# Kernel optimization log

Measured on AMD Instinct MI355X. Metric: run time of the kernel, lower is better.

## Reference

```python
import jax, jax.numpy as jnp
import numpy as np

THETA = 10000.0

def _rope_cos_sin(seq_len, head_dim, dtype=jnp.float32):
    # matches precompute_freqs_cis: freqs over even indices of head_dim
    inv = 1.0 / (THETA ** (jnp.arange(0, head_dim, 2, dtype=jnp.float32) / head_dim))  # [hd/2]
    ang = jnp.arange(seq_len, dtype=jnp.float32)[:, None] * inv[None, :]               # [S, hd/2]
    return jnp.cos(ang).astype(dtype), jnp.sin(ang).astype(dtype)

def _apply_rope(x, cos, sin):
    # x: [b, h, s, d]; pairs are interleaved (d r) with r=2 -> complex (even=real, odd=imag)
    xe = x[..., 0::2]
    xo = x[..., 1::2]
    re = xe * cos - xo * sin
    im = xe * sin + xo * cos
    # interleave back: [..., d/2, 2] -> [..., d]
    return jnp.stack([re, im], axis=-1).reshape(x.shape)

def setup_inputs() -> dict:
    key = jax.random.key(0)
    ks = jax.random.split(key, 8)
    B, S, D = 2, 2048, 1024
    s = 0.02
    return {
        "query": jax.random.normal(ks[0], (B, S, D), jnp.float32),
        "key": jax.random.normal(ks[1], (B, S, D), jnp.float32),
        "value": jax.random.normal(ks[2], (B, S, D), jnp.float32),
        "q_w": jax.random.normal(ks[3], (D, D), jnp.float32) * s,
        "q_b": jnp.zeros((D,), jnp.float32),
        "k_w": jax.random.normal(ks[4], (D, D), jnp.float32) * s,
        "k_b": jnp.zeros((D,), jnp.float32),
        "v_w": jax.random.normal(ks[5], (D, D), jnp.float32) * s,
        "v_b": jnp.zeros((D,), jnp.float32),
        "o_w": jax.random.normal(ks[6], (D, D), jnp.float32) * s,
        "o_b": jnp.zeros((D,), jnp.float32),
    }

def reference(query, key, value, q_w, q_b, k_w, k_b, v_w, v_b, o_w, o_b):
    H = 16
    B, S, D = query.shape
    hd = D // H
    scaling = hd ** -0.5

    def split_heads(x):  # [b, s, (h d)] -> [b, h, s, d]
        return x.reshape(B, -1, H, hd).transpose(0, 2, 1, 3)

    q = split_heads(query @ q_w.T + q_b)
    k = split_heads(key @ k_w.T + k_b)
    v = split_heads(value @ v_w.T + v_b)

    cos, sin = _rope_cos_sin(S, hd)
    q = _apply_rope(q, cos, sin)
    k = _apply_rope(k, cos, sin)

    scores = jnp.einsum('bhqd,bhkd->bhqk', q, k) * scaling  # [B,H,S,S]
    attn = jax.nn.softmax(scores, axis=-1)
    out = jnp.einsum('bhqk,bhkd->bhqd', attn, v)            # [B,H,S,hd]
    out = out.transpose(0, 2, 1, 3).reshape(B, S, D)
    return out @ o_w.T + o_b
```

## Files before the change

kernel.cpp:

```cpp
#include <hip/hip_runtime.h>
#include <math.h>

#define B_  2
#define S_  2048
#define D_  1024
#define H_  16
#define HD_ 64
#define M_  (B_*S_)

typedef __attribute__((ext_vector_type(8))) short bf16x8;
typedef __attribute__((ext_vector_type(4))) float f32x4;
typedef unsigned short ushort_t;

#define MFMA32 __builtin_amdgcn_mfma_f32_16x16x32_bf16

__device__ inline unsigned short f2bf(float x) {
    unsigned u = __float_as_uint(x);
    unsigned r = (u + 0x7fff + ((u >> 16) & 1)) >> 16;
    return (unsigned short)r;
}
__device__ inline void gload16(const ushort_t* g, ushort_t* l) {
    __builtin_amdgcn_global_load_lds(
        (const __attribute__((address_space(1))) unsigned*)g,
        (__attribute__((address_space(3))) unsigned*)l, 16, 0, 0);
}

__global__ __launch_bounds__(256) void prep(
    const float* __restrict__ qa, const float* __restrict__ ka,
    const float* __restrict__ va,
    const float* __restrict__ qw, const float* __restrict__ kw,
    const float* __restrict__ vw, const float* __restrict__ ow,
    ushort_t* __restrict__ qab, ushort_t* __restrict__ kab,
    ushort_t* __restrict__ vab,
    ushort_t* __restrict__ qwb, ushort_t* __restrict__ kwb,
    ushort_t* __restrict__ vwb, ushort_t* __restrict__ owb,
    float* __restrict__ cost, float* __restrict__ sint)
{
    const int z = blockIdx.y;
    const int i = blockIdx.x * 256 + threadIdx.x;
    if (z == 7) {
        if (blockIdx.x >= (S_ * 32) / 256) return;
        int s = i >> 5, w = i & 31;
        double inv = pow(10000.0, -((double)(2 * w) / (double)HD_));
        double ang = (double)s * inv;
        cost[i] = (float)cos(ang);
        sint[i] = (float)sin(ang);
        return;
    }
    const float* in;
    ushort_t* dst;
    int n4;
    switch (z) {
        case 0: in = qa; dst = qab; n4 = (M_ * D_) / 4; break;
        case 1: in = ka; dst = kab; n4 = (M_ * D_) / 4; break;
        case 2: in = va; dst = vab; n4 = (M_ * D_) / 4; break;
        case 3: in = qw; dst = qwb; n4 = (D_ * D_) / 4; break;
        case 4: in = kw; dst = kwb; n4 = (D_ * D_) / 4; break;
        case 5: in = vw; dst = vwb; n4 = (D_ * D_) / 4; break;
        default: in = ow; dst = owb; n4 = (D_ * D_) / 4; break;
    }
    if (i >= n4) return;
    float4 v = ((const float4*)in)[i];
    unsigned short h0 = f2bf(v.x), h1 = f2bf(v.y), h2 = f2bf(v.z), h3 = f2bf(v.w);
    ((uint2*)dst)[i] = make_uint2((unsigned)h0 | ((unsigned)h1 << 16),
                                  (unsigned)h2 | ((unsigned)h3 << 16));
}

__global__ __launch_bounds__(256, 3) void fused_qkv(
    const ushort_t* __restrict__ A0, const ushort_t* __restrict__ A1,
    const ushort_t* __restrict__ A2,
    const ushort_t* __restrict__ W0, const ushort_t* __restrict__ W1,
    const ushort_t* __restrict__ W2,
    const float* __restrict__ b0, const float* __restrict__ b1,
    const float* __restrict__ b2,
    ushort_t* __restrict__ O0, ushort_t* __restrict__ O1,
    ushort_t* __restrict__ O2,
    const float* __restrict__ cost, const float* __restrict__ sint)
{
    __shared__ ushort_t Ab[8192];
    __shared__ ushort_t Wb[8192];

    const int tid  = threadIdx.x;
    const int wq   = tid >> 6;
    const int lane = tid & 63;
    const int l16  = lane & 15;
    const int quad = lane >> 4;
    const int bm   = blockIdx.y * 128;
    const int bn   = blockIdx.x * 128;
    const int z    = blockIdx.z;

    const ushort_t* A = z == 0 ? A0 : z == 1 ? A1 : A2;
    const ushort_t* W = z == 0 ? W0 : z == 1 ? W1 : W2;
    const float* bias = z == 0 ? b0 : z == 1 ? b1 : b2;

    const int m16 = tid & 15;
    const int akq = (tid >> 4) & 3;
    const int tw  = tid >> 6;

    const ushort_t* gA0 = A + (size_t)(bm + tw * 16 + m16) * D_ + akq * 8;
    const ushort_t* gA1 = gA0 + (size_t)64 * D_;
    const ushort_t* gW0 = W + (size_t)(bn + tw * 16 + m16) * D_ + akq * 8;
    const ushort_t* gW1 = gW0 + (size_t)64 * D_;

    const int wm = wq >> 1, wn = wq & 1;

    f32x4 acc[4][4];
#pragma unroll
    for (int mt = 0; mt < 4; ++mt)
#pragma unroll
        for (int nt = 0; nt < 4; ++nt)
            acc[mt][nt] = (f32x4){0.f, 0.f, 0.f, 0.f};

    gload16(gA0, &Ab[tw * 512]);
    gload16(gA1, &Ab[(tw + 4) * 512]);
    gload16(gW0, &Wb[tw * 512]);
    gload16(gW1, &Wb[(tw + 4) * 512]);
    __syncthreads();

    for (int k0 = 0; k0 < D_; k0 += 32) {
        const int cur = (k0 >> 5) & 1;
        if (k0 + 32 < D_) {
            const int nxt = cur ^ 1;
            gload16(gA0 + k0 + 32, &Ab[nxt * 4096 + tw * 512]);
            gload16(gA1 + k0 + 32, &Ab[nxt * 4096 + (tw + 4) * 512]);
            gload16(gW0 + k0 + 32, &Wb[nxt * 4096 + tw * 512]);
            gload16(gW1 + k0 + 32, &Wb[nxt * 4096 + (tw + 4) * 512]);
        }
        const ushort_t* Abc = &Ab[cur * 4096];
        const ushort_t* Wbc = &Wb[cur * 4096];

        bf16x8 af[4], wf[4];
#pragma unroll
        for (int mt = 0; mt < 4; ++mt)
            af[mt] = *(const bf16x8*)&Abc[(wm * 4 + mt) * 512 + lane * 8];
#pragma unroll
        for (int nt = 0; nt < 4; ++nt)
            wf[nt] = *(const bf16x8*)&Wbc[(wn * 4 + nt) * 512 + lane * 8];
#pragma unroll
        for (int mt = 0; mt < 4; ++mt)
#pragma unroll
            for (int nt = 0; nt < 4; ++nt)
                acc[mt][nt] = MFMA32(af[mt], wf[nt], acc[mt][nt], 0, 0, 0);
        __syncthreads();
    }

    if (z == 0) {
        const float scale = 0.18033688011112042f;
#pragma unroll
        for (int mt = 0; mt < 4; ++mt) {
            int m = bm + wm * 64 + mt * 16 + quad * 4;
#pragma unroll
            for (int nt = 0; nt < 4; ++nt) {
                int n = bn + wn * 64 + nt * 16 + l16;
                float bb = bias[n];
                int h = n >> 6, d = n & 63, p = d >> 1;
#pragma unroll
                for (int r = 0; r < 4; ++r) {
                    int mm = m + r;
                    int s = mm & (S_ - 1), b = mm >> 11;
                    float x = acc[mt][nt][r] + bb;
                    float cs = cost[s * 32 + p], sn = sint[s * 32 + p];
                    float part = __shfl_xor(x, 1);
                    float y = (d & 1) ? (part * sn + x * cs)
                                      : (x * cs - part * sn);
                    O0[((size_t)(b * H_ + h) * S_ + s) * HD_ + d] = f2bf(y * scale);
                }
            }
        }
    } else if (z == 1) {
#pragma unroll
        for (int mt = 0; mt < 4; ++mt) {
            int m = bm + wm * 64 + mt * 16 + quad * 4;
#pragma unroll
            for (int nt = 0; nt < 4; ++nt) {
                int n = bn + wn * 64 + nt * 16 + l16;
                float bb = bias[n];
                int h = n >> 6, d = n & 63, p = d >> 1;
                int sub = ((d >> 5) & 1);
                int dq  = (d >> 3) & 3;
                int dj  = d & 7;
#pragma unroll
                for (int r = 0; r < 4; ++r) {
                    int mm = m + r;
                    int s = mm & (S_ - 1), b = mm >> 11;
                    float x = acc[mt][nt][r] + bb;
                    float cs = cost[s * 32 + p], sn = sint[s * 32 + p];
                    float part = __shfl_xor(x, 1);
                    float y = (d & 1) ? (part * sn + x * cs)
                                      : (x * cs - part * sn);
                    int kt  = s >> 5;
                    int st  = ((s >> 4) & 1) * 2 + sub;
                    size_t idx = ((size_t)(b * H_ + h) * 64 + kt) * 2048
                               + st * 512 + dq * 128 + (s & 15) * 8 + dj;
                    O1[idx] = f2bf(y);
                }
            }
        }
    } else {
#pragma unroll
        for (int mt = 0; mt < 4; ++mt) {
            int m = bm + wm * 64 + mt * 16 + quad * 4;
            int b = m >> 11, s0 = m & (S_ - 1);
            int vt = s0 >> 5;
            int kk = s0 & 31;
            int qd = (kk & 15) >> 2;
            int w0 = ((kk >> 4) & 1) * 4;
#pragma unroll
            for (int nt = 0; nt < 4; ++nt) {
                int n = bn + wn * 64 + nt * 16 + l16;
                float bb = bias[n];
                int h = n >> 6, d = n & 63;
                int mtv = d >> 4, dd = d & 15;
                unsigned short hh[4];
#pragma unroll
                for (int r = 0; r < 4; ++r)
                    hh[r] = f2bf(acc[mt][nt][r] + bb);
                size_t idx = ((size_t)(b * H_ + h) * 64 + vt) * 2048
                           + mtv * 512 + qd * 128 + dd * 8 + w0;
                *(uint2*)(O2 + idx) = make_uint2(
                    (unsigned)hh[0] | ((unsigned)hh[1] << 16),
                    (unsigned)hh[2] | ((unsigned)hh[3] << 16));
            }
        }
    }
}

__global__ __launch_bounds__(256, 2) void proj_o(
    const ushort_t* __restrict__ A, const ushort_t* __restrict__ W,
    const float* __restrict__ bias, float* __restrict__ outf)
{
    __shared__ ushort_t Ab[4096];
    __shared__ ushort_t Wb[8192];

    const int tid  = threadIdx.x;
    const int wq   = tid >> 6;
    const int lane = tid & 63;
    const int l16  = lane & 15;
    const int quad = lane >> 4;
    const int bm   = blockIdx.y * 64;
    const int bn   = blockIdx.x * 128;

    const int m16 = tid & 15;
    const int akq = (tid >> 4) & 3;
    const int tw  = tid >> 6;

    const ushort_t* gA  = A + (size_t)(bm + tw * 16 + m16) * D_ + akq * 8;
    const ushort_t* gW0 = W + (size_t)(bn + tw * 16 + m16) * D_ + akq * 8;
    const ushort_t* gW1 = gW0 + (size_t)64 * D_;

    const int wm = wq >> 1, wn = wq & 1;

    f32x4 acc[2][4];
#pragma unroll
    for (int mt = 0; mt < 2; ++mt)
#pragma unroll
        for (int nt = 0; nt < 4; ++nt)
            acc[mt][nt] = (f32x4){0.f, 0.f, 0.f, 0.f};

    gload16(gA,  &Ab[tw * 512]);
    gload16(gW0, &Wb[tw * 512]);
    gload16(gW1, &Wb[(tw + 4) * 512]);
    __syncthreads();

    for (int k0 = 0; k0 < D_; k0 += 32) {
        const int cur = (k0 >> 5) & 1;
        if (k0 + 32 < D_) {
            const int nxt = cur ^ 1;
            gload16(gA  + k0 + 32, &Ab[nxt * 2048 + tw * 512]);
            gload16(gW0 + k0 + 32, &Wb[nxt * 4096 + tw * 512]);
            gload16(gW1 + k0 + 32, &Wb[nxt * 4096 + (tw + 4) * 512]);
        }
        const ushort_t* Abc = &Ab[cur * 2048];
        const ushort_t* Wbc = &Wb[cur * 4096];

        bf16x8 af[2], wf[4];
#pragma unroll
        for (int mt = 0; mt < 2; ++mt)
            af[mt] = *(const bf16x8*)&Abc[(wm * 2 + mt) * 512 + lane * 8];
#pragma unroll
        for (int nt = 0; nt < 4; ++nt)
            wf[nt] = *(const bf16x8*)&Wbc[(wn * 4 + nt) * 512 + lane * 8];
#pragma unroll
        for (int mt = 0; mt < 2; ++mt)
#pragma unroll
            for (int nt = 0; nt < 4; ++nt)
                acc[mt][nt] = MFMA32(af[mt], wf[nt], acc[mt][nt], 0, 0, 0);
        __syncthreads();
    }

#pragma unroll
    for (int mt = 0; mt < 2; ++mt) {
        int m = bm + wm * 32 + mt * 16 + quad * 4;
#pragma unroll
        for (int nt = 0; nt < 4; ++nt) {
            int n = bn + wn * 64 + nt * 16 + l16;
            float bb = bias[n];
#pragma unroll
            for (int r = 0; r < 4; ++r)
                outf[(size_t)(m + r) * D_ + n] = acc[mt][nt][r] + bb;
        }
    }
}

__global__ __launch_bounds__(256, 2) void attn_mfma(
    const ushort_t* __restrict__ Q, const ushort_t* __restrict__ Kf,
    const ushort_t* __restrict__ Vf, ushort_t* __restrict__ AO)
{
    __shared__ __align__(16) unsigned char SM[33280 + 512];
    ushort_t* KS  = (ushort_t*)SM;
    ushort_t* VS  = (ushort_t*)(SM + 16384);
    float*    MRG = (float*)SM;
    float*    PSB = (float*)(SM + 33280);

    const int tid  = threadIdx.x;
    const int wq   = tid >> 6;
    const int lane = tid & 63;
    const int l16  = lane & 15;
    const int quad = lane >> 4;
    const int qg   = wq & 1;
    const int ks   = wq >> 1;
    const int bh   = blockIdx.y;
    const int q0   = blockIdx.x * 128 + qg * 64;

    bf16x8 qa[4][2];
#pragma unroll
    for (int nh = 0; nh < 4; ++nh)
#pragma unroll
        for (int c = 0; c < 2; ++c) {
            int row = q0 + nh * 16 + l16;
            qa[nh][c] = *(const bf16x8*)(Q + ((size_t)bh * S_ + row) * HD_
                                           + c * 32 + quad * 8);
        }

    f32x4 oacc[4][4];
    f32x4 osum[4];
#pragma unroll
    for (int nh = 0; nh < 4; ++nh) {
        osum[nh] = (f32x4){0.f, 0.f, 0.f, 0.f};
#pragma unroll
        for (int mt = 0; mt < 4; ++mt)
            oacc[nh][mt] = (f32x4){0.f, 0.f, 0.f, 0.f};
    }

    const bf16x8 ones8 = {(short)0x3F80, (short)0x3F80, (short)0x3F80,
                          (short)0x3F80, (short)0x3F80, (short)0x3F80,
                          (short)0x3F80, (short)0x3F80};

    const ushort_t* Kp = Kf + (size_t)bh * 64 * 2048;
    const ushort_t* Vp = Vf + (size_t)bh * 64 * 2048;

    gload16(Kp + tid * 8,        KS + tid * 8);
    gload16(Kp + 2048 + tid * 8, KS + 2048 + tid * 8);
    gload16(Vp + tid * 8,        VS + tid * 8);
    gload16(Vp + 2048 + tid * 8, VS + 2048 + tid * 8);
    Kp += 4096; Vp += 4096;
    __syncthreads();

    for (int i = 0; i < 32; ++i) {
        const int cur = i & 1;
        if (i < 31) {
            const int nxt = cur ^ 1;
            gload16(Kp + tid * 8,        KS + nxt * 4096 + tid * 8);
            gload16(Kp + 2048 + tid * 8, KS + nxt * 4096 + 2048 + tid * 8);
            gload16(Vp + tid * 8,        VS + nxt * 4096 + tid * 8);
            gload16(Vp + 2048 + tid * 8, VS + nxt * 4096 + 2048 + tid * 8);
            Kp += 4096; Vp += 4096;
        }
        const ushort_t* Kc = KS + cur * 4096 + ks * 2048;
        const ushort_t* Vc = VS + cur * 4096 + ks * 2048;

        bf16x8 kf[2][2];
#pragma unroll
        for (int g = 0; g < 2; ++g)
#pragma unroll
            for (int c = 0; c < 2; ++c)
                kf[g][c] = *(const bf16x8*)&Kc[(g * 2 + c) * 512 + lane * 8];

        f32x4 s[4][2];
#pragma unroll
        for (int nh = 0; nh < 4; ++nh)
#pragma unroll
            for (int g = 0; g < 2; ++g)
                s[nh][g] = (f32x4){0.f, 0.f, 0.f, 0.f};
#pragma unroll
        for (int c = 0; c < 2; ++c)
#pragma unroll
            for (int nh = 0; nh < 4; ++nh)
#pragma unroll
                for (int g = 0; g < 2; ++g)
                    s[nh][g] = MFMA32(kf[g][c], qa[nh][c], s[nh][g], 0, 0, 0);

        bf16x8 pb8[4];
#pragma unroll
        for (int nh = 0; nh < 4; ++nh) {
            float p00 = __builtin_exp2f(s[nh][0][0]);
            float p01 = __builtin_exp2f(s[nh][0][1]);
            float p02 = __builtin_exp2f(s[nh][0][2]);
            float p03 = __builtin_exp2f(s[nh][0][3]);
            float p10 = __builtin_exp2f(s[nh][1][0]);
            float p11 = __builtin_exp2f(s[nh][1][1]);
            float p12 = __builtin_exp2f(s[nh][1][2]);
            float p13 = __builtin_exp2f(s[nh][1][3]);
            union { bf16x8 v; unsigned u[4]; } t;
            t.u[0] = __builtin_amdgcn_perm(__float_as_uint(p01),
                                           __float_as_uint(p00), 0x07060302);
            t.u[1] = __builtin_amdgcn_perm(__float_as_uint(p03),
                                           __float_as_uint(p02), 0x07060302);
            t.u[2] = __builtin_amdgcn_perm(__float_as_uint(p11),
                                           __float_as_uint(p10), 0x07060302);
            t.u[3] = __builtin_amdgcn_perm(__float_as_uint(p13),
                                           __float_as_uint(p12), 0x07060302);
            pb8[nh] = t.v;
        }

#pragma unroll
        for (int mt = 0; mt < 4; ++mt) {
            bf16x8 vv = *(const bf16x8*)&Vc[mt * 512 + lane * 8];
#pragma unroll
            for (int nh = 0; nh < 4; ++nh)
                oacc[nh][mt] = MFMA32(vv, pb8[nh], oacc[nh][mt], 0, 0, 0);
        }
#pragma unroll
        for (int nh = 0; nh < 4; ++nh)
            osum[nh] = MFMA32(ones8, pb8[nh], osum[nh], 0, 0, 0);

        __syncthreads();
    }

    if (ks == 1) {
#pragma unroll
        for (int nh = 0; nh < 4; ++nh) {
#pragma unroll
            for (int mt = 0; mt < 4; ++mt)
#pragma unroll
                for (int r = 0; r < 4; ++r)
                    MRG[(qg * 64 + nh * 16 + l16) * 65 + mt * 16 + quad * 4 + r]
                        = oacc[nh][mt][r];
            if (quad == 0)
                PSB[qg * 64 + nh * 16 + l16] = osum[nh][0];
        }
    }
    __syncthreads();
    if (ks == 0) {
        const int b = bh >> 4, h = bh & 15;
#pragma unroll
        for (int nh = 0; nh < 4; ++nh) {
            float pst = osum[nh][0] + PSB[qg * 64 + nh * 16 + l16];
            float inv = 1.0f / pst;
            int q = q0 + nh * 16 + l16;
#pragma unroll
            for (int mt = 0; mt < 4; ++mt) {
                unsigned short hh[4];
#pragma unroll
                for (int r = 0; r < 4; ++r) {
                    float x = oacc[nh][mt][r]
                        + MRG[(qg * 64 + nh * 16 + l16) * 65 + mt * 16 + quad * 4 + r];
                    hh[r] = f2bf(x * inv);
                }
                size_t base = ((size_t)b * S_ + q) * D_ + h * HD_
                            + mt * 16 + quad * 4;
                *(uint2*)(AO + base) = make_uint2(
                    (unsigned)hh[0] | ((unsigned)hh[1] << 16),
                    (unsigned)hh[2] | ((unsigned)hh[3] << 16));
            }
        }
    }
}

extern "C" void kernel_launch(void* const* d_in, const int* in_sizes, int n_in,
                              void* d_out, int out_size, void* d_ws, size_t ws_size,
                              hipStream_t stream) {
    const float* query = (const float*)d_in[0];
    const float* key   = (const float*)d_in[1];
    const float* value = (const float*)d_in[2];
    const float* q_w   = (const float*)d_in[3];
    const float* q_b   = (const float*)d_in[4];
    const float* k_w   = (const float*)d_in[5];
    const float* k_b   = (const float*)d_in[6];
    const float* v_w   = (const float*)d_in[7];
    const float* v_b   = (const float*)d_in[8];
    const float* o_w   = (const float*)d_in[9];
    const float* o_b   = (const float*)d_in[10];
    float* out = (float*)d_out;

    const size_t NT = (size_t)M_ * D_;
    const size_t WT = (size_t)D_ * D_;
    ushort_t* p = (ushort_t*)d_ws;
    ushort_t* qa_b = p; p += NT;
    ushort_t* ka_b = p; p += NT;
    ushort_t* va_b = p; p += NT;
    ushort_t* wqb  = p; p += WT;
    ushort_t* wkb  = p; p += WT;
    ushort_t* wvb  = p; p += WT;
    ushort_t* wob  = p; p += WT;
    ushort_t* Qb   = p; p += NT;
    ushort_t* Kfr  = p; p += NT;
    ushort_t* Vfr  = p; p += NT;
    ushort_t* AO   = p; p += NT;
    float* cost = (float*)p;
    float* sint = cost + (size_t)S_ * 32;

    dim3 gp((unsigned)(NT / 4 / 256), 8);
    prep<<<gp, 256, 0, stream>>>(query, key, value, q_w, k_w, v_w, o_w,
                                 qa_b, ka_b, va_b, wqb, wkb, wvb, wob,
                                 cost, sint);

    dim3 gq(D_ / 128, M_ / 128, 3);
    fused_qkv<<<gq, 256, 0, stream>>>(
        qa_b, ka_b, va_b, wqb, wkb, wvb,
        q_b, k_b, v_b, Qb, Kfr, Vfr, cost, sint);

    dim3 agrid(S_ / 128, B_ * H_);
    attn_mfma<<<agrid, 256, 0, stream>>>(Qb, Kfr, Vfr, AO);

    dim3 go(D_ / 128, M_ / 64);
    proj_o<<<go, 256, 0, stream>>>(AO, wob, o_b, out);
}
```

Measured before the change: 254.2 us.

## Triple-buffer GEMM LDS loads with explicit vmcnt waits and MFMA priority hints

Both projection GEMMs move from double to triple-buffered LDS staging, issuing loads two k-steps ahead. They wait with explicit s_waitcnt vmcnt counts plus raw s_barrier instead of __syncthreads, so the next tiles' loads stay in flight across barriers. The attention kernel also uses partial vmcnt waits, raw barriers and s_setprio around its MFMA blocks, and pins the Q fragments in registers. The aim is to hide global-to-LDS latency and reduce barrier stalls, at the cost of more LDS (which may lower occupancy) and fragile hand-counted waitcnt values.

```diff
diff --git a/kernel.cpp b/kernel.cpp
--- a/kernel.cpp
+++ b/kernel.cpp
@@ -77,8 +77,8 @@
     ushort_t* __restrict__ O2,
     const float* __restrict__ cost, const float* __restrict__ sint)
 {
-    __shared__ ushort_t Ab[8192];
-    __shared__ ushort_t Wb[8192];
+    __shared__ ushort_t Ab[12288];
+    __shared__ ushort_t Wb[12288];
 
     const int tid  = threadIdx.x;
     const int wq   = tid >> 6;
@@ -111,23 +111,35 @@
         for (int nt = 0; nt < 4; ++nt)
             acc[mt][nt] = (f32x4){0.f, 0.f, 0.f, 0.f};
 
-    gload16(gA0, &Ab[tw * 512]);
-    gload16(gA1, &Ab[(tw + 4) * 512]);
-    gload16(gW0, &Wb[tw * 512]);
-    gload16(gW1, &Wb[(tw + 4) * 512]);
-    __syncthreads();
-
-    for (int k0 = 0; k0 < D_; k0 += 32) {
-        const int cur = (k0 >> 5) & 1;
-        if (k0 + 32 < D_) {
-            const int nxt = cur ^ 1;
-            gload16(gA0 + k0 + 32, &Ab[nxt * 4096 + tw * 512]);
-            gload16(gA1 + k0 + 32, &Ab[nxt * 4096 + (tw + 4) * 512]);
-            gload16(gW0 + k0 + 32, &Wb[nxt * 4096 + tw * 512]);
-            gload16(gW1 + k0 + 32, &Wb[nxt * 4096 + (tw + 4) * 512]);
-        }
-        const ushort_t* Abc = &Ab[cur * 4096];
-        const ushort_t* Wbc = &Wb[cur * 4096];
+    gload16(gA0,      &Ab[tw * 512]);
+    gload16(gA1,      &Ab[(tw + 4) * 512]);
+    gload16(gW0,      &Wb[tw * 512]);
+    gload16(gW1,      &Wb[(tw + 4) * 512]);
+    gload16(gA0 + 32, &Ab[4096 + tw * 512]);
+    gload16(gA1 + 32, &Ab[4096 + (tw + 4) * 512]);
+    gload16(gW0 + 32, &Wb[4096 + tw * 512]);
+    gload16(gW1 + 32, &Wb[4096 + (tw + 4) * 512]);
+
+    int bcur = 0;
+    for (int k = 0; k < 32; ++k) {
+        if (k < 30) {
+            int bnx = bcur + 2; if (bnx >= 3) bnx -= 3;
+            int ko = (k + 2) * 32;
+            gload16(gA0 + ko, &Ab[bnx * 4096 + tw * 512]);
+            gload16(gA1 + ko, &Ab[bnx * 4096 + (tw + 4) * 512]);
+            gload16(gW0 + ko, &Wb[bnx * 4096 + tw * 512]);
+            gload16(gW1 + ko, &Wb[bnx * 4096 + (tw + 4) * 512]);
+            asm volatile("s_waitcnt vmcnt(8)" ::: "memory");
+        } else if (k == 30) {
+            asm volatile("s_waitcnt vmcnt(4)" ::: "memory");
+        } else {
+            asm volatile("s_waitcnt vmcnt(0)" ::: "memory");
+        }
+        __builtin_amdgcn_s_barrier();
+        __builtin_amdgcn_sched_barrier(0);
+
+        const ushort_t* Abc = &Ab[bcur * 4096];
+        const ushort_t* Wbc = &Wb[bcur * 4096];
 
         bf16x8 af[4], wf[4];
 #pragma unroll
@@ -141,7 +153,10 @@
 #pragma unroll
             for (int nt = 0; nt < 4; ++nt)
                 acc[mt][nt] = MFMA32(af[mt], wf[nt], acc[mt][nt], 0, 0, 0);
-        __syncthreads();
+
+        __builtin_amdgcn_sched_barrier(0);
+        __builtin_amdgcn_s_barrier();
+        bcur += 1; if (bcur >= 3) bcur -= 3;
     }
 
     if (z == 0) {
@@ -229,8 +244,8 @@
     const ushort_t* __restrict__ A, const ushort_t* __restrict__ W,
     const float* __restrict__ bias, float* __restrict__ outf)
 {
-    __shared__ ushort_t Ab[4096];
-    __shared__ ushort_t Wb[8192];
+    __shared__ ushort_t Ab[6144];
+    __shared__ ushort_t Wb[12288];
 
     const int tid  = threadIdx.x;
     const int wq   = tid >> 6;
@@ -257,21 +272,32 @@
         for (int nt = 0; nt < 4; ++nt)
             acc[mt][nt] = (f32x4){0.f, 0.f, 0.f, 0.f};
 
-    gload16(gA,  &Ab[tw * 512]);
-    gload16(gW0, &Wb[tw * 512]);
-    gload16(gW1, &Wb[(tw + 4) * 512]);
-    __syncthreads();
-
-    for (int k0 = 0; k0 < D_; k0 += 32) {
-        const int cur = (k0 >> 5) & 1;
-        if (k0 + 32 < D_) {
-            const int nxt = cur ^ 1;
-            gload16(gA  + k0 + 32, &Ab[nxt * 2048 + tw * 512]);
-            gload16(gW0 + k0 + 32, &Wb[nxt * 4096 + tw * 512]);
-            gload16(gW1 + k0 + 32, &Wb[nxt * 4096 + (tw + 4) * 512]);
-        }
-        const ushort_t* Abc = &Ab[cur * 2048];
-        const ushort_t* Wbc = &Wb[cur * 4096];
+    gload16(gA,       &Ab[tw * 512]);
+    gload16(gW0,      &Wb[tw * 512]);
+    gload16(gW1,      &Wb[(tw + 4) * 512]);
+    gload16(gA + 32,  &Ab[2048 + tw * 512]);
+    gload16(gW0 + 32, &Wb[4096 + tw * 512]);
+    gload16(gW1 + 32, &Wb[4096 + (tw + 4) * 512]);
+
+    int bcur = 0;
+    for (int k = 0; k < 32; ++k) {
+        if (k < 30) {
+            int bnx = bcur + 2; if (bnx >= 3) bnx -= 3;
+            int ko = (k + 2) * 32;
+            gload16(gA  + ko, &Ab[bnx * 2048 + tw * 512]);
+            gload16(gW0 + ko, &Wb[bnx * 4096 + tw * 512]);
+            gload16(gW1 + ko, &Wb[bnx * 4096 + (tw + 4) * 512]);
+            asm volatile("s_waitcnt vmcnt(6)" ::: "memory");
+        } else if (k == 30) {
+            asm volatile("s_waitcnt vmcnt(3)" ::: "memory");
+        } else {
+            asm volatile("s_waitcnt vmcnt(0)" ::: "memory");
+        }
+        __builtin_amdgcn_s_barrier();
+        __builtin_amdgcn_sched_barrier(0);
+
+        const ushort_t* Abc = &Ab[bcur * 2048];
+        const ushort_t* Wbc = &Wb[bcur * 4096];
 
         bf16x8 af[2], wf[4];
 #pragma unroll
@@ -285,7 +311,10 @@
 #pragma unroll
             for (int nt = 0; nt < 4; ++nt)
                 acc[mt][nt] = MFMA32(af[mt], wf[nt], acc[mt][nt], 0, 0, 0);
-        __syncthreads();
+
+        __builtin_amdgcn_sched_barrier(0);
+        __builtin_amdgcn_s_barrier();
+        bcur += 1; if (bcur >= 3) bcur -= 3;
     }
 
 #pragma unroll
@@ -331,6 +360,11 @@
             qa[nh][c] = *(const bf16x8*)(Q + ((size_t)bh * S_ + row) * HD_
                                            + c * 32 + quad * 8);
         }
+#pragma unroll
+    for (int nh = 0; nh < 4; ++nh)
+#pragma unroll
+        for (int c = 0; c < 2; ++c)
+            asm volatile("" : "+v"(qa[nh][c]));
 
     f32x4 oacc[4][4];
     f32x4 osum[4];
@@ -346,26 +380,31 @@
                           (short)0x3F80, (short)0x3F80, (short)0x3F80,
                           (short)0x3F80, (short)0x3F80};
 
-    const ushort_t* Kp = Kf + (size_t)bh * 64 * 2048;
-    const ushort_t* Vp = Vf + (size_t)bh * 64 * 2048;
-
-    gload16(Kp + tid * 8,        KS + tid * 8);
-    gload16(Kp + 2048 + tid * 8, KS + 2048 + tid * 8);
-    gload16(Vp + tid * 8,        VS + tid * 8);
-    gload16(Vp + 2048 + tid * 8, VS + 2048 + tid * 8);
-    Kp += 4096; Vp += 4096;
-    __syncthreads();
+    const ushort_t* Kbase = Kf + (size_t)bh * 64 * 2048;
+    const ushort_t* Vbase = Vf + (size_t)bh * 64 * 2048;
+
+    gload16(Kbase + tid * 8,        KS + tid * 8);
+    gload16(Kbase + 2048 + tid * 8, KS + 2048 + tid * 8);
+    gload16(Vbase + tid * 8,        VS + tid * 8);
+    gload16(Vbase + 2048 + tid * 8, VS + 2048 + tid * 8);
 
     for (int i = 0; i < 32; ++i) {
         const int cur = i & 1;
         if (i < 31) {
-            const int nxt = cur ^ 1;
-            gload16(Kp + tid * 8,        KS + nxt * 4096 + tid * 8);
-            gload16(Kp + 2048 + tid * 8, KS + nxt * 4096 + 2048 + tid * 8);
-            gload16(Vp + tid * 8,        VS + nxt * 4096 + tid * 8);
-            gload16(Vp + 2048 + tid * 8, VS + nxt * 4096 + 2048 + tid * 8);
-            Kp += 4096; Vp += 4096;
-        }
+            const int nb = cur ^ 1;
+            const ushort_t* Kq = Kbase + (size_t)(i + 1) * 4096;
+            const ushort_t* Vq = Vbase + (size_t)(i + 1) * 4096;
+            gload16(Kq + tid * 8,        KS + nb * 4096 + tid * 8);
+            gload16(Kq + 2048 + tid * 8, KS + nb * 4096 + 2048 + tid * 8);
+            gload16(Vq + tid * 8,        VS + nb * 4096 + tid * 8);
+            gload16(Vq + 2048 + tid * 8, VS + nb * 4096 + 2048 + tid * 8);
+            asm volatile("s_waitcnt vmcnt(4)" ::: "memory");
+        } else {
+            asm volatile("s_waitcnt vmcnt(0)" ::: "memory");
+        }
+        __builtin_amdgcn_s_barrier();
+        __builtin_amdgcn_sched_barrier(0);
+
         const ushort_t* Kc = KS + cur * 4096 + ks * 2048;
         const ushort_t* Vc = VS + cur * 4096 + ks * 2048;
 
@@ -382,6 +421,7 @@
 #pragma unroll
             for (int g = 0; g < 2; ++g)
                 s[nh][g] = (f32x4){0.f, 0.f, 0.f, 0.f};
+        __builtin_amdgcn_s_setprio(1);
 #pragma unroll
         for (int c = 0; c < 2; ++c)
 #pragma unroll
@@ -389,6 +429,7 @@
 #pragma unroll
                 for (int g = 0; g < 2; ++g)
                     s[nh][g] = MFMA32(kf[g][c], qa[nh][c], s[nh][g], 0, 0, 0);
+        __builtin_amdgcn_s_setprio(0);
 
         bf16x8 pb8[4];
 #pragma unroll
@@ -413,6 +454,7 @@
             pb8[nh] = t.v;
         }
 
+        __builtin_amdgcn_s_setprio(1);
 #pragma unroll
         for (int mt = 0; mt < 4; ++mt) {
             bf16x8 vv = *(const bf16x8*)&Vc[mt * 512 + lane * 8];
@@ -423,8 +465,10 @@
 #pragma unroll
         for (int nh = 0; nh < 4; ++nh)
             osum[nh] = MFMA32(ones8, pb8[nh], osum[nh], 0, 0, 0);
-
-        __syncthreads();
+        __builtin_amdgcn_s_setprio(0);
+
+        __builtin_amdgcn_sched_barrier(0);
+        __builtin_amdgcn_s_barrier();
     }
 
     if (ks == 1) {
```

After: 251.3 us. No clear change (-1.1%).
